# Kernel optimization log

Hardware: AMD Instinct MI355X
Metric: run time of the kernel (lower is better)

## Reference

```python
import jax, jax.numpy as jnp
import numpy as np
from jax import lax

B, T = 64, 200
NUM_C, DIM_S, SIZE_M = 2000, 128, 50


def setup_inputs() -> dict:
    key = jax.random.key(0)
    ks = jax.random.split(key, 12)
    d = {}
    d['skill'] = jax.random.randint(ks[0], (B, T), 0, NUM_C)
    d['answer'] = jax.random.randint(ks[1], (B, T), 0, 2)
    s = 1.0 / np.sqrt(DIM_S)
    d['k_emb'] = jax.random.normal(ks[2], (NUM_C + 1, DIM_S), jnp.float32)
    d['v_emb'] = jax.random.normal(ks[3], (2 * NUM_C + 1, DIM_S), jnp.float32)
    # kaiming_normal on [size_m, dim_s]: std = sqrt(2/dim_s)
    d['Mk'] = jax.random.normal(ks[4], (SIZE_M, DIM_S), jnp.float32) * np.sqrt(2.0 / DIM_S)
    d['Mv0'] = jax.random.normal(ks[5], (SIZE_M, DIM_S), jnp.float32) * np.sqrt(2.0 / DIM_S)
    d['f_W'] = jax.random.normal(ks[6], (DIM_S, 2 * DIM_S), jnp.float32) * (1.0 / np.sqrt(2 * DIM_S))
    d['f_b'] = jnp.zeros((DIM_S,), jnp.float32)
    d['p_W'] = jax.random.normal(ks[7], (NUM_C, DIM_S), jnp.float32) * s
    d['p_b'] = jnp.zeros((NUM_C,), jnp.float32)
    d['e_W'] = jax.random.normal(ks[8], (DIM_S, DIM_S), jnp.float32) * s
    d['e_b'] = jnp.zeros((DIM_S,), jnp.float32)
    d['a_W'] = jax.random.normal(ks[9], (DIM_S, DIM_S), jnp.float32) * s
    d['a_b'] = jnp.zeros((DIM_S,), jnp.float32)
    return d


def reference(skill, answer, k_emb, v_emb, Mk, Mv0, f_W, f_b, p_W, p_b, e_W, e_b, a_W, a_b):
    num_c = p_W.shape[0]
    bsz = skill.shape[0]
    answer_x = jnp.where(answer == 2, 1, answer)
    x = skill + num_c * answer_x                       # [B,T]
    k = k_emb[skill]                                   # [B,T,D]
    v = v_emb[x]                                       # [B,T,D]
    w = jax.nn.softmax(jnp.einsum('btd,md->btm', k, Mk), axis=-1)   # [B,T,M]
    e = jax.nn.sigmoid(jnp.einsum('btd,ed->bte', v, e_W) + e_b)      # [B,T,D]
    a = jnp.tanh(jnp.einsum('btd,ed->bte', v, a_W) + a_b)            # [B,T,D]

    Mv_init = jnp.broadcast_to(Mv0, (bsz,) + Mv0.shape)              # [B,M,D]

    def step(Mvt, inp):
        et, at, wt = inp                               # [B,D],[B,D],[B,M]
        # read uses pre-update memory (Mv[:, :-1] in the torch code)
        read = jnp.einsum('bm,bmd->bd', wt, Mvt)
        Mvt_new = Mvt * (1.0 - wt[:, :, None] * et[:, None, :]) + wt[:, :, None] * at[:, None, :]
        return Mvt_new, read

    _, reads = lax.scan(step, Mv_init,
                        (e.transpose(1, 0, 2), a.transpose(1, 0, 2), w.transpose(1, 0, 2)))
    reads = reads.transpose(1, 0, 2)                   # [B,T,D]

    f = jnp.tanh(jnp.concatenate([reads, k], axis=-1) @ f_W.T + f_b)  # [B,T,D]
    p = jax.nn.sigmoid(f @ p_W.T + p_b)                # [B,T,num_c] (dropout is identity at eval)
    p = p[:, :-1, :]
    next_skill = skill[:, 1:]                          # [B,T-1]
    idx = jnp.minimum(next_skill, num_c - 1)
    pred = jnp.take_along_axis(p, idx[..., None], axis=-1)[..., 0]
    pred = jnp.where(next_skill < num_c, pred, 0.0)    # index num_c -> zero row in torch one_hot
    return pred
```

## Files before the change

kernel.cpp:

```cpp
#include <hip/hip_runtime.h>
#include <math.h>

#define Bsz 64
#define Tn 200
#define NUMC 2000
#define DS 128
#define SM 50
#define NTOK (Bsz*Tn)
#define WG2 10
#define MPG2 5

typedef __attribute__((ext_vector_type(8))) short bfrag;
typedef __attribute__((ext_vector_type(4))) float f32x4;
typedef __attribute__((ext_vector_type(4))) unsigned int u32x4;

__device__ __forceinline__ unsigned short f2bf(float x) {
    unsigned int u = __builtin_bit_cast(unsigned int, x);
    u = u + 0x7fffu + ((u >> 16) & 1u);
    return (unsigned short)(u >> 16);
}
__device__ __forceinline__ unsigned int pack2(float a, float b) {
    return (unsigned int)f2bf(a) | ((unsigned int)f2bf(b) << 16);
}
__device__ __forceinline__ bfrag mk_frag(f32x4 x, f32x4 y) {
    u32x4 t;
    t[0] = pack2(x[0], x[1]); t[1] = pack2(x[2], x[3]);
    t[2] = pack2(y[0], y[1]); t[3] = pack2(y[2], y[3]);
    return __builtin_bit_cast(bfrag, t);
}

__device__ __forceinline__ void load_group(const bfrag* __restrict__ B, int nt0, int L, bfrag bf[4][4]) {
    #pragma unroll
    for (int t = 0; t < 4; t++)
        #pragma unroll
        for (int ki = 0; ki < 4; ki++)
            bf[t][ki] = B[(size_t)((nt0 + t) * 4 + ki) * 64 + L];
}
__device__ __forceinline__ void mfma_group(const bfrag A[4], const bfrag bf[4][4], f32x4 acc[4]) {
    #pragma unroll
    for (int ki = 0; ki < 4; ki++)
        #pragma unroll
        for (int t = 0; t < 4; t++)
            acc[t] = __builtin_amdgcn_mfma_f32_16x16x32_bf16(A[ki], bf[t][ki], acc[t], 0, 0, 0);
}

__global__ __launch_bounds__(256) void k0_cast(
    const float* __restrict__ eW, const float* __restrict__ aW,
    const float* __restrict__ fW, const float* __restrict__ Mk,
    unsigned int* __restrict__ BeaU, unsigned int* __restrict__ BkmU,
    unsigned int* __restrict__ Bf0U)
{
    const int g = blockIdx.x * 256 + threadIdx.x;
    if (g >= 9216) return;
    int gm, mat;
    unsigned int* dst;
    if (g < 4096)      { mat = 0; gm = g;        dst = BeaU; }
    else if (g < 7168) { mat = 1; gm = g - 4096; dst = BkmU; }
    else               { mat = 2; gm = g - 7168; dst = Bf0U; }
    const int nt = gm >> 8, r = gm & 255, ki = r >> 6, L = r & 63;
    const int n = nt * 16 + (L & 15);
    const int k = ki * 32 + (L >> 4) * 8;

    const float* src = nullptr;
    if (mat == 0) {
        src = (n < 128) ? (eW + (size_t)n * DS + k) : (aW + (size_t)(n - 128) * DS + k);
    } else if (mat == 1) {
        if (n < 128)      src = fW + (size_t)n * (2 * DS) + DS + k;
        else if (n < 128 + SM) src = Mk + (size_t)(n - 128) * DS + k;
    } else {
        src = fW + (size_t)n * (2 * DS) + k;
    }
    float v[8];
    #pragma unroll
    for (int j = 0; j < 8; j++) v[j] = src ? src[j] : 0.f;
    u32x4 o;
    o[0] = pack2(v[0], v[1]); o[1] = pack2(v[2], v[3]);
    o[2] = pack2(v[4], v[5]); o[3] = pack2(v[6], v[7]);
    ((u32x4*)dst)[gm] = o;
}

__global__ __launch_bounds__(256) void k1_gemm(
    const int* __restrict__ skill, const int* __restrict__ answer,
    const float* __restrict__ k_emb, const float* __restrict__ v_emb,
    const unsigned int* __restrict__ BeaU, const unsigned int* __restrict__ BkmU,
    const float* __restrict__ eB, const float* __restrict__ aB,
    float* __restrict__ w_buf, float* __restrict__ e_buf,
    float* __restrict__ a_buf, float* __restrict__ kp_buf)
{
    const int tid = threadIdx.x;
    const int w = tid >> 6, L = tid & 63, L15 = L & 15, quad = L >> 4;
    const int tok0 = blockIdx.x * 64;
    const int tokA = tok0 + 16 * w + L15;
    const int tokD0 = tok0 + 16 * w + quad * 4;

    const int s  = skill[tokA];
    const int an = answer[tokA];
    const int ax = (an == 2) ? 1 : an;
    const float* vp = v_emb + ((size_t)(s + NUMC * ax)) * DS + quad * 8;
    const float* kp = k_emb + (size_t)s * DS + quad * 8;

    bfrag Vf[4], Kf[4];
    #pragma unroll
    for (int ki = 0; ki < 4; ki++) {
        const f32x4* a = (const f32x4*)(vp + ki * 32);
        Vf[ki] = mk_frag(a[0], a[1]);
        const f32x4* b = (const f32x4*)(kp + ki * 32);
        Kf[ki] = mk_frag(b[0], b[1]);
    }

    const bfrag* Bea = (const bfrag*)BeaU;
    const bfrag* Bkm = (const bfrag*)BkmU;

    __shared__ float wl[64][52];

    {
        bfrag bfA[4][4], bfB[4][4];
        load_group(Bea, 0, L, bfA);
        load_group(Bea, 4, L, bfB);

        #define EA_EPI_E(NT0, ACC)                                              \
            { _Pragma("unroll")                                                 \
              for (int t = 0; t < 4; t++) {                                     \
                const int n = (NT0 + t) * 16 + L15;                             \
                const float bias = eB[n];                                       \
                _Pragma("unroll")                                               \
                for (int reg = 0; reg < 4; reg++)                               \
                    e_buf[(size_t)(tokD0 + reg) * DS + n] =                     \
                        1.f / (1.f + expf(-(ACC[t][reg] + bias)));              \
              } }
        #define EA_EPI_A(NT0, ACC)                                              \
            { _Pragma("unroll")                                                 \
              for (int t = 0; t < 4; t++) {                                     \
                const int n = (NT0 + t) * 16 + L15 - 128;                       \
                const float bias = aB[n];                                       \
                _Pragma("unroll")                                               \
                for (int reg = 0; reg < 4; reg++)                               \
                    a_buf[(size_t)(tokD0 + reg) * DS + n] =                     \
                        tanhf(ACC[t][reg] + bias);                              \
              } }

        f32x4 acc[4];
        #pragma unroll
        for (int t = 0; t < 4; t++) acc[t] = (f32x4){0.f,0.f,0.f,0.f};
        mfma_group(Vf, bfA, acc);
        load_group(Bea, 8, L, bfA);
        EA_EPI_E(0, acc);

        #pragma unroll
        for (int t = 0; t < 4; t++) acc[t] = (f32x4){0.f,0.f,0.f,0.f};
        mfma_group(Vf, bfB, acc);
        load_group(Bea, 12, L, bfB);
        EA_EPI_E(4, acc);

        #pragma unroll
        for (int t = 0; t < 4; t++) acc[t] = (f32x4){0.f,0.f,0.f,0.f};
        mfma_group(Vf, bfA, acc);
        EA_EPI_A(8, acc);

        #pragma unroll
        for (int t = 0; t < 4; t++) acc[t] = (f32x4){0.f,0.f,0.f,0.f};
        mfma_group(Vf, bfB, acc);
        EA_EPI_A(12, acc);
    }

    {
        bfrag bfA[4][4], bfB[4][4];
        load_group(Bkm, 0, L, bfA);
        load_group(Bkm, 4, L, bfB);

        f32x4 acc[4];
        #pragma unroll
        for (int t = 0; t < 4; t++) acc[t] = (f32x4){0.f,0.f,0.f,0.f};
        mfma_group(Kf, bfA, acc);
        load_group(Bkm, 8, L, bfA);
        #pragma unroll
        for (int t = 0; t < 4; t++) {
            const int n = t * 16 + L15;
            #pragma unroll
            for (int reg = 0; reg < 4; reg++)
                kp_buf[(size_t)(tokD0 + reg) * DS + n] = acc[t][reg];
        }

        #pragma unroll
        for (int t = 0; t < 4; t++) acc[t] = (f32x4){0.f,0.f,0.f,0.f};
        mfma_group(Kf, bfB, acc);
        #pragma unroll
        for (int t = 0; t < 4; t++) {
            const int n = (4 + t) * 16 + L15;
            #pragma unroll
            for (int reg = 0; reg < 4; reg++)
                kp_buf[(size_t)(tokD0 + reg) * DS + n] = acc[t][reg];
        }

        #pragma unroll
        for (int t = 0; t < 4; t++) acc[t] = (f32x4){0.f,0.f,0.f,0.f};
        mfma_group(Kf, bfA, acc);
        #pragma unroll
        for (int t = 0; t < 4; t++) {
            const int c = (8 + t) * 16 + L15 - 128;
            if (c < SM) {
                #pragma unroll
                for (int reg = 0; reg < 4; reg++)
                    wl[16 * w + quad * 4 + reg][c] = acc[t][reg];
            }
        }
    }
    __syncthreads();
    if (tid < 64) {
        float mx = -1e30f;
        for (int m = 0; m < SM; m++) mx = fmaxf(mx, wl[tid][m]);
        float sum = 0.f;
        float ex[SM];
        for (int m = 0; m < SM; m++) { ex[m] = expf(wl[tid][m] - mx); sum += ex[m]; }
        const float inv = 1.f / sum;
        float* wp = w_buf + (size_t)(tok0 + tid) * SM;
        for (int m = 0; m < SM; m++) wp[m] = ex[m] * inv;
    }
}

__global__ __launch_bounds__(64) void k2_scan(
    const float* __restrict__ w_buf, const float* __restrict__ e_buf,
    const float* __restrict__ a_buf, const float* __restrict__ Mv0,
    float* __restrict__ part_buf)
{
    const int bi   = blockIdx.x;
    const int b    = bi / (2*WG2);
    const int r    = bi % (2*WG2);
    const int dh   = r / WG2;
    const int mg   = r % WG2;
    const int lane = threadIdx.x;
    const int d    = dh*64 + lane;
    const int m0   = mg * MPG2;
    const int base = b * Tn;

    float Mv[MPG2];
    #pragma unroll
    for (int m = 0; m < MPG2; m++) Mv[m] = Mv0[(size_t)(m0+m)*DS + d];

    float* pout = part_buf + (size_t)mg * NTOK * DS;

    float se[4][2], sa[4][2], sw[4][2][MPG2];

    #define LOADST(ST, T)                                                      \
        { const int tc_ = ((T) < Tn) ? (T) : 0;                                \
          _Pragma("unroll")                                                    \
          for (int q_ = 0; q_ < 2; q_++) {                                     \
              const int tf_ = base + tc_ + q_;                                 \
              se[ST][q_] = e_buf[(size_t)tf_*DS + d];                          \
              sa[ST][q_] = a_buf[(size_t)tf_*DS + d];                          \
              _Pragma("unroll")                                                \
              for (int m_ = 0; m_ < MPG2; m_++)                                \
                  sw[ST][q_][m_] = w_buf[(size_t)tf_*SM + m0 + m_];            \
          } }

    LOADST(0, 0) LOADST(1, 2) LOADST(2, 4) LOADST(3, 6)

    for (int i = 0; i < 25; i++) {
        const int tb = i * 8;
        #pragma unroll
        for (int sub = 0; sub < 4; sub++) {
            const int t0 = tb + sub * 2;
            #pragma unroll
            for (int q = 0; q < 2; q++) {
                const float ev = se[sub][q], av = sa[sub][q];
                float rd = 0.f;
                #pragma unroll
                for (int m = 0; m < MPG2; m++) {
                    const float wm = sw[sub][q][m];
                    rd = fmaf(wm, Mv[m], rd);
                    Mv[m] = fmaf(-wm, fmaf(ev, Mv[m], -av), Mv[m]);
                }
                pout[(size_t)(base + t0 + q)*DS + d] = rd;
            }
            LOADST(sub, t0 + 8)
        }
    }
}

__global__ __launch_bounds__(256) void k3_gemm(
    const float* __restrict__ part_buf, const float* __restrict__ kp_buf,
    const unsigned int* __restrict__ Bf0U, const float* __restrict__ fB,
    const float* __restrict__ pW, const float* __restrict__ pB,
    const int* __restrict__ skill, float* __restrict__ out)
{
    const int tid = threadIdx.x;
    const int w = tid >> 6, L = tid & 63, L15 = L & 15, quad = L >> 4;
    const int tok0 = blockIdx.x * 64;
    const int tokA = tok0 + 16 * w + L15;
    const int tokD0 = tok0 + 16 * w + quad * 4;

    const bfrag* Bf0 = (const bfrag*)Bf0U;
    bfrag bfA[4][4], bfB[4][4];
    load_group(Bf0, 0, L, bfA);
    load_group(Bf0, 4, L, bfB);

    bfrag Rf[4];
    #pragma unroll
    for (int ki = 0; ki < 4; ki++) {
        const float* p0 = part_buf + (size_t)tokA * DS + ki * 32 + quad * 8;
        f32x4 x = (f32x4){0.f,0.f,0.f,0.f}, y = (f32x4){0.f,0.f,0.f,0.f};
        #pragma unroll
        for (int g = 0; g < WG2; g++) {
            const f32x4* q4 = (const f32x4*)(p0 + (size_t)g * NTOK * DS);
            x = x + q4[0]; y = y + q4[1];
        }
        Rf[ki] = mk_frag(x, y);
    }

    float f[4][8];
    f32x4 acc[4];

    #pragma unroll
    for (int t = 0; t < 4; t++) acc[t] = (f32x4){0.f,0.f,0.f,0.f};
    mfma_group(Rf, bfA, acc);
    #pragma unroll
    for (int t = 0; t < 4; t++) {
        const int n = t * 16 + L15;
        const float fb = fB[n];
        #pragma unroll
        for (int reg = 0; reg < 4; reg++)
            f[reg][t] = tanhf(acc[t][reg] + kp_buf[(size_t)(tokD0 + reg) * DS + n] + fb);
    }

    #pragma unroll
    for (int t = 0; t < 4; t++) acc[t] = (f32x4){0.f,0.f,0.f,0.f};
    mfma_group(Rf, bfB, acc);
    #pragma unroll
    for (int t = 0; t < 4; t++) {
        const int n = (4 + t) * 16 + L15;
        const float fb = fB[n];
        #pragma unroll
        for (int reg = 0; reg < 4; reg++)
            f[reg][4 + t] = tanhf(acc[t][reg] + kp_buf[(size_t)(tokD0 + reg) * DS + n] + fb);
    }

    #pragma unroll
    for (int reg = 0; reg < 4; reg++) {
        const int tok = tokD0 + reg;
        const int t = tok % Tn;
        const bool act = (t < Tn - 1);
        int sn = 0, ix = 0;
        float contrib = 0.f;
        if (act) {
            sn = skill[tok + 1];
            ix = (sn < NUMC) ? sn : (NUMC - 1);
            const float* pr = pW + (size_t)ix * DS + L15;
            #pragma unroll
            for (int nt = 0; nt < 8; nt++)
                contrib = fmaf(f[reg][nt], pr[nt * 16], contrib);
        }
        #pragma unroll
        for (int msk = 1; msk <= 8; msk <<= 1)
            contrib += __shfl_xor(contrib, msk);
        if (act && L15 == 0) {
            const float val = contrib + pB[ix];
            const float prd = (sn < NUMC) ? (1.f / (1.f + expf(-val))) : 0.f;
            out[(size_t)(tok / Tn) * (Tn - 1) + t] = prd;
        }
    }
}

extern "C" void kernel_launch(void* const* d_in, const int* in_sizes, int n_in,
                              void* d_out, int out_size, void* d_ws, size_t ws_size,
                              hipStream_t stream)
{
    const int*   skill  = (const int*)  d_in[0];
    const int*   answer = (const int*)  d_in[1];
    const float* k_emb  = (const float*)d_in[2];
    const float* v_emb  = (const float*)d_in[3];
    const float* Mk     = (const float*)d_in[4];
    const float* Mv0    = (const float*)d_in[5];
    const float* f_W    = (const float*)d_in[6];
    const float* f_b    = (const float*)d_in[7];
    const float* p_W    = (const float*)d_in[8];
    const float* p_b    = (const float*)d_in[9];
    const float* e_W    = (const float*)d_in[10];
    const float* e_b    = (const float*)d_in[11];
    const float* a_W    = (const float*)d_in[12];
    const float* a_b    = (const float*)d_in[13];
    float* out = (float*)d_out;

    float* ws       = (float*)d_ws;
    float* w_buf    = ws;
    float* e_buf    = w_buf    + (size_t)NTOK*SM;
    float* a_buf    = e_buf    + (size_t)NTOK*DS;
    float* kp_buf   = a_buf    + (size_t)NTOK*DS;
    float* part_buf = kp_buf   + (size_t)NTOK*DS;
    unsigned int* BeaU = (unsigned int*)(part_buf + (size_t)WG2*NTOK*DS);
    unsigned int* BkmU = BeaU + 4096 * 4;
    unsigned int* Bf0U = BkmU + 3072 * 4;

    k0_cast<<<36, 256, 0, stream>>>(e_W, a_W, f_W, Mk, BeaU, BkmU, Bf0U);
    k1_gemm<<<NTOK/64, 256, 0, stream>>>(skill, answer, k_emb, v_emb,
        BeaU, BkmU, e_b, a_b, w_buf, e_buf, a_buf, kp_buf);
    k2_scan<<<Bsz*2*WG2, 64, 0, stream>>>(w_buf, e_buf, a_buf, Mv0, part_buf);
    k3_gemm<<<NTOK/64, 256, 0, stream>>>(part_buf, kp_buf, Bf0U, f_b,
        p_W, p_b, skill, out);
}
```

Measured before the change: 156.5 us.

## Split k1 into single-wave e/a and key blocks, shrink k3 blocks, use fast transcendentals

k1 now launches one 64-thread wave per 16 tokens. Half the blocks compute the e/a projections and the other half compute the key projection plus the memory softmax, so the two GEMM halves run in parallel rather than back to back. k3 also moves to one-wave blocks over 16 tokens, giving more blocks and finer scheduling. expf/tanhf/division are replaced with exp2 and rcp hardware intrinsics, which are cheaper but slightly less accurate. Each block now reloads the bf16 weight fragments for fewer tokens, which adds L2 traffic.

New measurement: 140.6 us. 1.11x faster.

```diff
diff --git a/kernel.cpp b/kernel.cpp
--- a/kernel.cpp
+++ b/kernel.cpp
@@ -28,6 +28,11 @@
     t[2] = pack2(y[0], y[1]); t[3] = pack2(y[2], y[3]);
     return __builtin_bit_cast(bfrag, t);
 }
+
+__device__ __forceinline__ float fast_exp(float x)  { return __builtin_amdgcn_exp2f(x * 1.44269504f); }
+__device__ __forceinline__ float fast_rcp(float x)  { return __builtin_amdgcn_rcpf(x); }
+__device__ __forceinline__ float fast_sigmoid(float x) { return fast_rcp(1.f + fast_exp(-x)); }
+__device__ __forceinline__ float fast_tanh(float x) { return 1.f - 2.f * fast_rcp(fast_exp(2.f * x) + 1.f); }
 
 __device__ __forceinline__ void load_group(const bfrag* __restrict__ B, int nt0, int L, bfrag bf[4][4]) {
     #pragma unroll
@@ -79,7 +84,7 @@
     ((u32x4*)dst)[gm] = o;
 }
 
-__global__ __launch_bounds__(256) void k1_gemm(
+__global__ __launch_bounds__(64) void k1_gemm(
     const int* __restrict__ skill, const int* __restrict__ answer,
     const float* __restrict__ k_emb, const float* __restrict__ v_emb,
     const unsigned int* __restrict__ BeaU, const unsigned int* __restrict__ BkmU,
@@ -87,86 +92,100 @@
     float* __restrict__ w_buf, float* __restrict__ e_buf,
     float* __restrict__ a_buf, float* __restrict__ kp_buf)
 {
-    const int tid = threadIdx.x;
-    const int w = tid >> 6, L = tid & 63, L15 = L & 15, quad = L >> 4;
-    const int tok0 = blockIdx.x * 64;
-    const int tokA = tok0 + 16 * w + L15;
-    const int tokD0 = tok0 + 16 * w + quad * 4;
-
-    const int s  = skill[tokA];
-    const int an = answer[tokA];
-    const int ax = (an == 2) ? 1 : an;
-    const float* vp = v_emb + ((size_t)(s + NUMC * ax)) * DS + quad * 8;
-    const float* kp = k_emb + (size_t)s * DS + quad * 8;
-
-    bfrag Vf[4], Kf[4];
-    #pragma unroll
-    for (int ki = 0; ki < 4; ki++) {
-        const f32x4* a = (const f32x4*)(vp + ki * 32);
-        Vf[ki] = mk_frag(a[0], a[1]);
-        const f32x4* b = (const f32x4*)(kp + ki * 32);
-        Kf[ki] = mk_frag(b[0], b[1]);
-    }
-
-    const bfrag* Bea = (const bfrag*)BeaU;
-    const bfrag* Bkm = (const bfrag*)BkmU;
-
-    __shared__ float wl[64][52];
-
-    {
+    const int bid = blockIdx.x;
+    const int L = threadIdx.x, L15 = L & 15, quad = L >> 4;
+
+    if (bid < NTOK/16) {
+        const int tok0 = bid * 16;
+        const int tokA = tok0 + L15;
+        const int tokD0 = tok0 + quad * 4;
+
+        const bfrag* Bea = (const bfrag*)BeaU;
         bfrag bfA[4][4], bfB[4][4];
         load_group(Bea, 0, L, bfA);
         load_group(Bea, 4, L, bfB);
 
-        #define EA_EPI_E(NT0, ACC)                                              \
-            { _Pragma("unroll")                                                 \
-              for (int t = 0; t < 4; t++) {                                     \
-                const int n = (NT0 + t) * 16 + L15;                             \
-                const float bias = eB[n];                                       \
-                _Pragma("unroll")                                               \
-                for (int reg = 0; reg < 4; reg++)                               \
-                    e_buf[(size_t)(tokD0 + reg) * DS + n] =                     \
-                        1.f / (1.f + expf(-(ACC[t][reg] + bias)));              \
-              } }
-        #define EA_EPI_A(NT0, ACC)                                              \
-            { _Pragma("unroll")                                                 \
-              for (int t = 0; t < 4; t++) {                                     \
-                const int n = (NT0 + t) * 16 + L15 - 128;                       \
-                const float bias = aB[n];                                       \
-                _Pragma("unroll")                                               \
-                for (int reg = 0; reg < 4; reg++)                               \
-                    a_buf[(size_t)(tokD0 + reg) * DS + n] =                     \
-                        tanhf(ACC[t][reg] + bias);                              \
-              } }
+        const int s  = skill[tokA];
+        const int an = answer[tokA];
+        const int ax = (an == 2) ? 1 : an;
+        const float* vp = v_emb + ((size_t)(s + NUMC * ax)) * DS + quad * 8;
+        bfrag Vf[4];
+        #pragma unroll
+        for (int ki = 0; ki < 4; ki++) {
+            const f32x4* a = (const f32x4*)(vp + ki * 32);
+            Vf[ki] = mk_frag(a[0], a[1]);
+        }
 
         f32x4 acc[4];
         #pragma unroll
         for (int t = 0; t < 4; t++) acc[t] = (f32x4){0.f,0.f,0.f,0.f};
         mfma_group(Vf, bfA, acc);
         load_group(Bea, 8, L, bfA);
-        EA_EPI_E(0, acc);
+        #pragma unroll
+        for (int t = 0; t < 4; t++) {
+            const int n = t * 16 + L15;
+            const float bias = eB[n];
+            #pragma unroll
+            for (int reg = 0; reg < 4; reg++)
+                e_buf[(size_t)(tokD0 + reg) * DS + n] = fast_sigmoid(acc[t][reg] + bias);
+        }
 
         #pragma unroll
         for (int t = 0; t < 4; t++) acc[t] = (f32x4){0.f,0.f,0.f,0.f};
         mfma_group(Vf, bfB, acc);
         load_group(Bea, 12, L, bfB);
-        EA_EPI_E(4, acc);
+        #pragma unroll
+        for (int t = 0; t < 4; t++) {
+            const int n = (4 + t) * 16 + L15;
+            const float bias = eB[n];
+            #pragma unroll
+            for (int reg = 0; reg < 4; reg++)
+                e_buf[(size_t)(tokD0 + reg) * DS + n] = fast_sigmoid(acc[t][reg] + bias);
+        }
 
         #pragma unroll
         for (int t = 0; t < 4; t++) acc[t] = (f32x4){0.f,0.f,0.f,0.f};
         mfma_group(Vf, bfA, acc);
-        EA_EPI_A(8, acc);
+        #pragma unroll
+        for (int t = 0; t < 4; t++) {
+            const int n = t * 16 + L15;
+            const float bias = aB[n];
+            #pragma unroll
+            for (int reg = 0; reg < 4; reg++)
+                a_buf[(size_t)(tokD0 + reg) * DS + n] = fast_tanh(acc[t][reg] + bias);
+        }
 
         #pragma unroll
         for (int t = 0; t < 4; t++) acc[t] = (f32x4){0.f,0.f,0.f,0.f};
         mfma_group(Vf, bfB, acc);
-        EA_EPI_A(12, acc);
-    }
-
-    {
+        #pragma unroll
+        for (int t = 0; t < 4; t++) {
+            const int n = (4 + t) * 16 + L15;
+            const float bias = aB[n];
+            #pragma unroll
+            for (int reg = 0; reg < 4; reg++)
+                a_buf[(size_t)(tokD0 + reg) * DS + n] = fast_tanh(acc[t][reg] + bias);
+        }
+    } else {
+        const int tok0 = (bid - NTOK/16) * 16;
+        const int tokA = tok0 + L15;
+        const int tokD0 = tok0 + quad * 4;
+
+        const bfrag* Bkm = (const bfrag*)BkmU;
         bfrag bfA[4][4], bfB[4][4];
         load_group(Bkm, 0, L, bfA);
         load_group(Bkm, 4, L, bfB);
+
+        const int s = skill[tokA];
+        const float* kp = k_emb + (size_t)s * DS + quad * 8;
+        bfrag Kf[4];
+        #pragma unroll
+        for (int ki = 0; ki < 4; ki++) {
+            const f32x4* b = (const f32x4*)(kp + ki * 32);
+            Kf[ki] = mk_frag(b[0], b[1]);
+        }
+
+        __shared__ float wl[16][52];
 
         f32x4 acc[4];
         #pragma unroll
@@ -201,20 +220,20 @@
             if (c < SM) {
                 #pragma unroll
                 for (int reg = 0; reg < 4; reg++)
-                    wl[16 * w + quad * 4 + reg][c] = acc[t][reg];
+                    wl[quad * 4 + reg][c] = acc[t][reg];
             }
         }
-    }
-    __syncthreads();
-    if (tid < 64) {
-        float mx = -1e30f;
-        for (int m = 0; m < SM; m++) mx = fmaxf(mx, wl[tid][m]);
-        float sum = 0.f;
-        float ex[SM];
-        for (int m = 0; m < SM; m++) { ex[m] = expf(wl[tid][m] - mx); sum += ex[m]; }
-        const float inv = 1.f / sum;
-        float* wp = w_buf + (size_t)(tok0 + tid) * SM;
-        for (int m = 0; m < SM; m++) wp[m] = ex[m] * inv;
+        __syncthreads();
+        if (L < 16) {
+            float mx = -1e30f;
+            for (int m = 0; m < SM; m++) mx = fmaxf(mx, wl[L][m]);
+            float sum = 0.f;
+            float ex[SM];
+            for (int m = 0; m < SM; m++) { ex[m] = fast_exp(wl[L][m] - mx); sum += ex[m]; }
+            const float inv = fast_rcp(sum);
+            float* wp = w_buf + (size_t)(tok0 + L) * SM;
+            for (int m = 0; m < SM; m++) wp[m] = ex[m] * inv;
+        }
     }
 }
 
@@ -277,17 +296,16 @@
     }
 }
 
-__global__ __launch_bounds__(256) void k3_gemm(
+__global__ __launch_bounds__(64) void k3_gemm(
     const float* __restrict__ part_buf, const float* __restrict__ kp_buf,
     const unsigned int* __restrict__ Bf0U, const float* __restrict__ fB,
     const float* __restrict__ pW, const float* __restrict__ pB,
     const int* __restrict__ skill, float* __restrict__ out)
 {
-    const int tid = threadIdx.x;
-    const int w = tid >> 6, L = tid & 63, L15 = L & 15, quad = L >> 4;
-    const int tok0 = blockIdx.x * 64;
-    const int tokA = tok0 + 16 * w + L15;
-    const int tokD0 = tok0 + 16 * w + quad * 4;
+    const int L = threadIdx.x, L15 = L & 15, quad = L >> 4;
+    const int tok0 = blockIdx.x * 16;
+    const int tokA = tok0 + L15;
+    const int tokD0 = tok0 + quad * 4;
 
     const bfrag* Bf0 = (const bfrag*)Bf0U;
     bfrag bfA[4][4], bfB[4][4];
@@ -319,7 +337,7 @@
         const float fb = fB[n];
         #pragma unroll
         for (int reg = 0; reg < 4; reg++)
-            f[reg][t] = tanhf(acc[t][reg] + kp_buf[(size_t)(tokD0 + reg) * DS + n] + fb);
+            f[reg][t] = fast_tanh(acc[t][reg] + kp_buf[(size_t)(tokD0 + reg) * DS + n] + fb);
     }
 
     #pragma unroll
@@ -331,7 +349,7 @@
         const float fb = fB[n];
         #pragma unroll
         for (int reg = 0; reg < 4; reg++)
-            f[reg][4 + t] = tanhf(acc[t][reg] + kp_buf[(size_t)(tokD0 + reg) * DS + n] + fb);
+            f[reg][4 + t] = fast_tanh(acc[t][reg] + kp_buf[(size_t)(tokD0 + reg) * DS + n] + fb);
     }
 
     #pragma unroll
@@ -354,7 +372,7 @@
             contrib += __shfl_xor(contrib, msk);
         if (act && L15 == 0) {
             const float val = contrib + pB[ix];
-            const float prd = (sn < NUMC) ? (1.f / (1.f + expf(-val))) : 0.f;
+            const float prd = (sn < NUMC) ? fast_sigmoid(val) : 0.f;
             out[(size_t)(tok / Tn) * (Tn - 1) + t] = prd;
         }
     }
@@ -391,9 +409,9 @@
     unsigned int* Bf0U = BkmU + 3072 * 4;
 
     k0_cast<<<36, 256, 0, stream>>>(e_W, a_W, f_W, Mk, BeaU, BkmU, Bf0U);
-    k1_gemm<<<NTOK/64, 256, 0, stream>>>(skill, answer, k_emb, v_emb,
+    k1_gemm<<<2*(NTOK/16), 64, 0, stream>>>(skill, answer, k_emb, v_emb,
         BeaU, BkmU, e_b, a_b, w_buf, e_buf, a_buf, kp_buf);
     k2_scan<<<Bsz*2*WG2, 64, 0, stream>>>(w_buf, e_buf, a_buf, Mv0, part_buf);
-    k3_gemm<<<NTOK/64, 256, 0, stream>>>(part_buf, kp_buf, Bf0U, f_b,
+    k3_gemm<<<NTOK/16, 64, 0, stream>>>(part_buf, kp_buf, Bf0U, f_b,
         p_W, p_b, skill, out);
 }
```
